# Performance work log

Hardware: AMD Instinct MI355X
Metric: run time of the kernel (lower is better)

Reference implementation:

```python
import jax, jax.numpy as jnp
from jax import lax
import numpy as np

B, C, H, W = 8, 192, 56, 56
N = H * W
K_CLUSTERS = 16   # num_centroids
K_NBRS = 9        # kNN neighbors
FACTOR = 2
COUT = C * FACTOR # hidden channels of graph conv
CPE_K = 7         # depthwise CPE kernel (odd)


def setup_inputs() -> dict:
    key = jax.random.key(0)
    ks = jax.random.split(key, 12)
    s = 0.02
    return {
        "x": jax.random.normal(ks[0], (B, C, H, W), jnp.float32),
        "labels": jax.random.randint(ks[1], (B, N), 0, K_CLUSTERS, jnp.int32),
        "cpe_w": jax.random.normal(ks[2], (C, 1, CPE_K, CPE_K), jnp.float32) * s,
        "cpe_b": jnp.zeros((C,), jnp.float32),
        "fc1_w": jax.random.normal(ks[3], (C, C), jnp.float32) * s,
        "fc1_b": jnp.zeros((C,), jnp.float32),
        "nn_v_w": jax.random.normal(ks[4], (2 * C, COUT), jnp.float32) * s,
        "nn_v_b": jnp.zeros((COUT,), jnp.float32),
        "nn_c_w": jax.random.normal(ks[5], (2 * C, COUT), jnp.float32) * s,
        "nn_c_b": jnp.zeros((COUT,), jnp.float32),
        "fc2_w": jax.random.normal(ks[6], (COUT, C), jnp.float32) * s,
        "fc2_b": jnp.zeros((C,), jnp.float32),
    }


def reference(x, labels, cpe_w, cpe_b, fc1_w, fc1_b, nn_v_w, nn_v_b,
              nn_c_w, nn_c_b, fc2_w, fc2_b):
    Bx, Cx, Hx, Wx = x.shape
    n = Hx * Wx
    shortcut = x
    # --- Conditional Position Encoding: depthwise conv + residual ---
    pe = lax.conv_general_dilated(
        x, cpe_w, (1, 1), "SAME", feature_group_count=Cx,
        dimension_numbers=("NCHW", "OIHW", "NCHW"))
    x = pe + cpe_b[None, :, None, None] + x
    # --- fc1: 1x1 conv ---
    xf = jnp.einsum("bchw,cd->bdhw", x, fc1_w) + fc1_b[None, :, None, None]
    xn = xf.reshape(Bx, Cx, n).transpose(0, 2, 1)  # [B,N,C]
    # --- organize_and_map: stable sort nodes by cluster label ---
    order = jnp.argsort(labels, axis=1)            # sorted pos -> orig idx (stable)
    mapping = jnp.argsort(order, axis=1)           # orig idx -> sorted pos
    xs = jnp.take_along_axis(xn, order[:, :, None], axis=1)  # [B,N,C]
    ls = jnp.take_along_axis(labels, order, axis=1)          # [B,N]
    # --- kNN on l2-normalized feats, restricted to same cluster ---
    xe = xs / jnp.maximum(jnp.linalg.norm(xs, axis=-1, keepdims=True), 1e-12)
    sq = jnp.sum(xe * xe, axis=-1)                 # [B,N]
    d2 = sq[:, :, None] + sq[:, None, :] - 2.0 * jnp.einsum("bnc,bmc->bnm", xe, xe)
    same = ls[:, :, None] == ls[:, None, :]        # [B,N,N] cluster mask
    d2 = jnp.where(same, d2, jnp.inf)
    _, nbr = lax.top_k(-d2, K_NBRS)                # [B,N,k] nearest in-cluster
    valid = jnp.take_along_axis(same, nbr, axis=2) # False when cluster < k
    # --- vertex edge conv: max_j MLP([x_i, x_j - x_i]) ---
    xj = jax.vmap(lambda xb, nb: xb[nb])(xs, nbr)  # [B,N,k,C]
    xi = xs[:, :, None, :]
    msg = jnp.concatenate([jnp.broadcast_to(xi, xj.shape), xj - xi], axis=-1)
    h = jax.nn.gelu(msg @ nn_v_w + nn_v_b)         # [B,N,k,COUT]
    h = jnp.where(valid[..., None], h, -jnp.inf)   # self is always valid
    hv = jnp.max(h, axis=2)                        # [B,N,COUT]
    # --- centroid edge conv over cluster centers (fully connected per image) ---
    onehot = (ls[:, :, None] == jnp.arange(K_CLUSTERS)[None, None, :]).astype(xs.dtype)
    cnt = jnp.maximum(onehot.sum(axis=1), 1.0)     # [B,K]
    cen = jnp.einsum("bnk,bnc->bkc", onehot, xs) / cnt[:, :, None]
    ci = cen[:, :, None, :]
    cj = cen[:, None, :, :]
    cmsg = jnp.concatenate(
        [jnp.broadcast_to(ci, (Bx, K_CLUSTERS, K_CLUSTERS, Cx)), cj - ci], axis=-1)
    hc = jnp.max(jax.nn.gelu(cmsg @ nn_c_w + nn_c_b), axis=2)  # [B,K,COUT]
    hcn = jax.vmap(lambda hb, lb: hb[lb])(hc, ls)  # scatter center feat to nodes
    hn = hv + hcn                                  # [B,N,COUT]
    # --- unshuffle back to original raster order ---
    out_nodes = jnp.take_along_axis(hn, mapping[:, :, None], axis=1)
    # --- fc2: 1x1 conv back to C, residual ---
    y = out_nodes @ fc2_w + fc2_b                  # [B,N,C]
    y = y.transpose(0, 2, 1).reshape(Bx, Cx, Hx, Wx)
    return y + shortcut
```

## Files before the change

kernel.cpp:

```cpp
#include <hip/hip_runtime.h>
#include <math.h>

#define NB 8
#define NC 192
#define NH 56
#define NW 56
#define NN 3136
#define NK 16
#define KNB 9
#define NCOUT 384
#define LPMAX 320
#define DSTRIDE 320
#define DSLOT (320 * 320)

#define FLT_INF __builtin_inff()

typedef short s16x8 __attribute__((ext_vector_type(8)));
typedef _Float16 f16x8 __attribute__((ext_vector_type(8)));
typedef float f32x4 __attribute__((ext_vector_type(4)));
typedef unsigned short us8 __attribute__((ext_vector_type(8)));
typedef unsigned short us4 __attribute__((ext_vector_type(4)));

__device__ __forceinline__ float gelu_t(float x) {
    const float k0 = 0.7978845608028654f;
    float u = k0 * (x + 0.044715f * x * x * x);
    float t = tanhf(u);
    return 0.5f * x * (1.0f + t);
}

__device__ __forceinline__ unsigned short f2bf(float f) {
    unsigned u = __float_as_uint(f);
    u += 0x7fff + ((u >> 16) & 1);
    return (unsigned short)(u >> 16);
}

__device__ __forceinline__ float bf2f(unsigned short h) {
    return __uint_as_float(((unsigned)h) << 16);
}

__global__ void order_kernel(const int* __restrict__ labels, int* __restrict__ order,
                             int* __restrict__ mapping, int* __restrict__ lsv,
                             int* __restrict__ cntk, int* __restrict__ offk) {
    int b = blockIdx.x >> 4;
    int k = blockIdx.x & 15;
    int lane = threadIdx.x;
    const int* lb = labels + (size_t)b * NN;
    int cntLess = 0, cntEq = 0;
    for (int n0 = 0; n0 < NN; n0 += 64) {
        int lab = lb[n0 + lane] & 15;
        cntLess += __popcll(__ballot(lab < k));
        cntEq += __popcll(__ballot(lab == k));
    }
    int base = cntLess;
    int run = 0;
    for (int n0 = 0; n0 < NN; n0 += 64) {
        int n = n0 + lane;
        int lab = lb[n] & 15;
        bool p = (lab == k);
        unsigned long long mask = __ballot(p);
        int rank = __popcll(mask & ((1ull << lane) - 1ull));
        if (p) {
            int pos = base + run + rank;
            order[b * NN + pos] = n;
            mapping[b * NN + n] = pos;
            lsv[b * NN + pos] = k;
        }
        run += __popcll(mask);
    }
    if (lane == 0) {
        offk[b * NK + k] = base;
        cntk[b * NK + k] = cntEq;
    }
}

__global__ __launch_bounds__(256) void conv_kernel(const float* __restrict__ X,
                                                   const float* __restrict__ W7,
                                                   const float* __restrict__ bias,
                                                   unsigned short* __restrict__ xpe) {
    __shared__ float tile[62 * 62];
    __shared__ float wl[49];
    int bc = blockIdx.x;
    int c = bc % NC;
    const float* Xp = X + (size_t)bc * NN;
    int tid = threadIdx.x;
    if (tid < 49) wl[tid] = W7[(size_t)c * 49 + tid];
    for (int idx = tid; idx < 62 * 62; idx += 256) {
        int ty = idx / 62, tx = idx % 62;
        int gy = ty - 3, gx = tx - 3;
        float v = 0.0f;
        if (gy >= 0 && gy < NH && gx >= 0 && gx < NW) v = Xp[gy * NW + gx];
        tile[idx] = v;
    }
    __syncthreads();
    float cb = bias[c];
    for (int g = tid; g < (NN / 4); g += 256) {
        int y = g / (NW / 4), x0 = (g % (NW / 4)) * 4;
        float a0 = 0.f, a1 = 0.f, a2 = 0.f, a3 = 0.f;
#pragma unroll
        for (int dy = 0; dy < 7; ++dy) {
            const float* tr = &tile[(y + dy) * 62 + x0];
#pragma unroll
            for (int dx = 0; dx < 7; ++dx) {
                float wv = wl[dy * 7 + dx];
                a0 += tr[dx] * wv;
                a1 += tr[dx + 1] * wv;
                a2 += tr[dx + 2] * wv;
                a3 += tr[dx + 3] * wv;
            }
        }
        const float* rr = &tile[(y + 3) * 62 + x0 + 3];
        us4 o;
        o[0] = f2bf(a0 + cb + rr[0]);
        o[1] = f2bf(a1 + cb + rr[1]);
        o[2] = f2bf(a2 + cb + rr[2]);
        o[3] = f2bf(a3 + cb + rr[3]);
        *(us4*)(xpe + (size_t)bc * NN + y * NW + x0) = o;
    }
}

__global__ void wcvt_all_kernel(const float* __restrict__ Wf1, const float* __restrict__ Wv,
                                const float* __restrict__ Wf2, unsigned short* __restrict__ wf1,
                                unsigned short* __restrict__ wfpmq,
                                unsigned short* __restrict__ wfq,
                                unsigned short* __restrict__ wf2) {
    int z = blockIdx.z, nt = blockIdx.x, kc = blockIdx.y;
    const float* W;
    unsigned short* Bf;
    int ldw, rowoff, KC, NT;
    bool diff = false;
    if (z == 0) { W = Wf1; Bf = wf1; ldw = NC; rowoff = 0; KC = 6; NT = 3; }
    else if (z == 1) { W = Wv; Bf = wfpmq; ldw = NCOUT; rowoff = 0; KC = 6; NT = 6; diff = true; }
    else if (z == 2) { W = Wv; Bf = wfq; ldw = NCOUT; rowoff = NC; KC = 6; NT = 6; }
    else { W = Wf2; Bf = wf2; ldw = NC; rowoff = 0; KC = 12; NT = 3; }
    if (nt >= NT || kc >= KC) return;
    int tid = threadIdx.x;
    int c = tid >> 6, l = tid & 63;
    int n = l & 15, q = l >> 4;
    int col = nt * 64 + c * 16 + n;
    int krow = rowoff + kc * 32 + q * 8;
    unsigned short pack[8];
#pragma unroll
    for (int j = 0; j < 8; ++j) {
        float v = W[(size_t)(krow + j) * ldw + col];
        if (diff) v -= W[(size_t)(NC + krow + j) * ldw + col];
        pack[j] = f2bf(v);
    }
    *(us8*)(Bf + ((((size_t)nt * KC + kc) * 4 + c) * 64 + l) * 8) = *(const us8*)pack;
}

__global__ __launch_bounds__(256) void tcvt_kernel(const unsigned short* __restrict__ xpe,
                                                   unsigned short* __restrict__ Af) {
    __shared__ unsigned short t[32][72];
    int b = blockIdx.z, kc = blockIdx.y, n0 = blockIdx.x * 64;
    int tid = threadIdx.x;
    int cl = tid >> 3, nl = (tid & 7) * 8;
    const unsigned short* src = xpe + ((size_t)b * NC + kc * 32 + cl) * NN + n0 + nl;
    *(us8*)&t[cl][nl] = *(const us8*)src;
    __syncthreads();
    int w = tid >> 6, l = tid & 63;
    int m = l & 15, q = l >> 4;
    int nloc = w * 16 + m;
    unsigned short pack[8];
#pragma unroll
    for (int j = 0; j < 8; ++j) pack[j] = t[q * 8 + j][nloc];
    int sg = blockIdx.x * 4 + w;
    *(us8*)(Af + (size_t)b * NN * NC + (((size_t)sg * 6 + kc) * 64 + l) * 8) =
        *(const us8*)pack;
}

template <int KC>
__global__ __launch_bounds__(256) void gemm_mfma(const unsigned short* __restrict__ Af,
                                                 size_t aStride,
                                                 const unsigned short* __restrict__ Bf,
                                                 const float* __restrict__ bias,
                                                 float* __restrict__ C, size_t cStride,
                                                 int ldc, unsigned short* __restrict__ Cfrag,
                                                 const int* __restrict__ rowmap) {
    int b = blockIdx.z;
    int w = threadIdx.x >> 6, lane = threadIdx.x & 63;
    int sg = blockIdx.y * 4 + w;
    int n0 = blockIdx.x * 64;
    const unsigned short* Ap = Af + (size_t)b * aStride + ((size_t)sg * KC * 64 + lane) * 8;
    const unsigned short* Bp = Bf + ((size_t)blockIdx.x * KC * 256 + lane) * 8;
    f32x4 acc[4] = {};
#pragma unroll
    for (int kc = 0; kc < KC; ++kc) {
        s16x8 a = *(const s16x8*)(Ap + kc * 512);
#pragma unroll
        for (int c = 0; c < 4; ++c) {
            s16x8 bv = *(const s16x8*)(Bp + kc * 2048 + c * 512);
            acc[c] = __builtin_amdgcn_mfma_f32_16x16x32_bf16(a, bv, acc[c], 0, 0, 0);
        }
    }
    int col0 = lane & 15, rq = lane >> 4;
    float* Cb = C + (size_t)b * cStride;
    int kcd = ldc >> 5;
#pragma unroll
    for (int r = 0; r < 4; ++r) {
        int grow = sg * 16 + rq * 4 + r;
        int orow = rowmap ? rowmap[(size_t)b * NN + grow] : grow;
#pragma unroll
        for (int c = 0; c < 4; ++c) {
            int col = n0 + c * 16 + col0;
            float v = acc[c][r];
            if (bias) v += bias[col];
            Cb[(size_t)orow * ldc + col] = v;
            if (Cfrag) {
                int s2 = orow >> 4, m2 = orow & 15;
                int kc2 = col >> 5, q2 = (col >> 3) & 3, j2 = col & 7;
                Cfrag[(size_t)b * cStride +
                      (((size_t)s2 * kcd + kc2) * 64 + q2 * 16 + m2) * 8 + j2] = f2bf(v);
            }
        }
    }
}

template <int KC>
__global__ __launch_bounds__(256) void gemm_mfma_h(const unsigned short* __restrict__ Af,
                                                   size_t aStride,
                                                   const unsigned short* __restrict__ Bf,
                                                   unsigned short* __restrict__ C,
                                                   size_t cStride, int ldc) {
    int b = blockIdx.z;
    int w = threadIdx.x >> 6, lane = threadIdx.x & 63;
    int sg = blockIdx.y * 4 + w;
    int n0 = blockIdx.x * 64;
    const unsigned short* Ap = Af + (size_t)b * aStride + ((size_t)sg * KC * 64 + lane) * 8;
    const unsigned short* Bp = Bf + ((size_t)blockIdx.x * KC * 256 + lane) * 8;
    f32x4 acc[4] = {};
#pragma unroll
    for (int kc = 0; kc < KC; ++kc) {
        s16x8 a = *(const s16x8*)(Ap + kc * 512);
#pragma unroll
        for (int c = 0; c < 4; ++c) {
            s16x8 bv = *(const s16x8*)(Bp + kc * 2048 + c * 512);
            acc[c] = __builtin_amdgcn_mfma_f32_16x16x32_bf16(a, bv, acc[c], 0, 0, 0);
        }
    }
    int col0 = lane & 15, rq = lane >> 4;
    unsigned short* Cb = C + (size_t)b * cStride;
#pragma unroll
    for (int r = 0; r < 4; ++r) {
        int grow = sg * 16 + rq * 4 + r;
#pragma unroll
        for (int c = 0; c < 4; ++c) {
            int col = n0 + c * 16 + col0;
            Cb[(size_t)grow * ldc + col] = f2bf(acc[c][r]);
        }
    }
}

__global__ void norm_kernel(const float* __restrict__ xs, float* __restrict__ rinv,
                            float* __restrict__ sqv) {
    int row = blockIdx.x * 4 + (threadIdx.x >> 6);
    int lane = threadIdx.x & 63;
    const float* p = xs + (size_t)row * NC;
    float v0 = p[lane], v1 = p[lane + 64], v2 = p[lane + 128];
    float s = v0 * v0 + v1 * v1 + v2 * v2;
#pragma unroll
    for (int m = 32; m; m >>= 1) s += __shfl_xor(s, m, 64);
    float nrm = fmaxf(sqrtf(s), 1e-12f);
    float ri = 1.0f / nrm;
    float e0 = v0 * ri, e1 = v1 * ri, e2 = v2 * ri;
    float s2 = e0 * e0 + e1 * e1 + e2 * e2;
#pragma unroll
    for (int m = 32; m; m >>= 1) s2 += __shfl_xor(s2, m, 64);
    if (lane == 0) {
        rinv[row] = ri;
        sqv[row] = s2;
    }
}

__global__ __launch_bounds__(384) void xe_cvt_kernel(const float* __restrict__ xs,
                                                     const float* __restrict__ rinv,
                                                     const int* __restrict__ offk,
                                                     const int* __restrict__ cntk,
                                                     _Float16* __restrict__ xef) {
    int b = blockIdx.z, k = blockIdx.y, strip = blockIdx.x;
    int bk = b * NK + k;
    int base = offk[bk], L = cntk[bk];
    if (strip * 16 >= L) return;
    int kc = threadIdx.x >> 6, l = threadIdx.x & 63;
    int m = l & 15, q = l >> 4;
    int rl = strip * 16 + m;
    int row = base + (rl < L ? rl : L - 1);
    float rv = rinv[(size_t)b * NN + row];
    const float* src = xs + ((size_t)b * NN + row) * NC + kc * 32 + q * 8;
    float4 v0 = *(const float4*)src;
    float4 v1 = *(const float4*)(src + 4);
    f16x8 pack;
    pack[0] = (_Float16)(v0.x * rv);
    pack[1] = (_Float16)(v0.y * rv);
    pack[2] = (_Float16)(v0.z * rv);
    pack[3] = (_Float16)(v0.w * rv);
    pack[4] = (_Float16)(v1.x * rv);
    pack[5] = (_Float16)(v1.y * rv);
    pack[6] = (_Float16)(v1.z * rv);
    pack[7] = (_Float16)(v1.w * rv);
    *(f16x8*)(xef + (size_t)bk * (20 * 6 * 512) + (((size_t)strip * 6 + kc) * 64 + l) * 8) =
        pack;
}

__global__ __launch_bounds__(256) void gram_kernel(const _Float16* __restrict__ xef,
                                                   const float* __restrict__ sqv,
                                                   const int* __restrict__ offk,
                                                   const int* __restrict__ cntk,
                                                   float* __restrict__ D) {
    int bk = blockIdx.z;
    int b = bk >> 4;
    int base = offk[bk], L = cntk[bk];
    int ti = blockIdx.x, tj = blockIdx.y;
    if (ti * 64 >= L || tj * 64 >= L) return;
    int w = threadIdx.x >> 6, lane = threadIdx.x & 63;
    const _Float16* Xf = xef + (size_t)bk * (20 * 6 * 512);
    const _Float16* Ap = Xf + (((size_t)(ti * 4 + w) * 6) * 64 + lane) * 8;
    f32x4 acc[4] = {};
#pragma unroll
    for (int kc = 0; kc < 6; ++kc) {
        f16x8 a = *(const f16x8*)(Ap + kc * 512);
#pragma unroll
        for (int js = 0; js < 4; ++js) {
            f16x8 bv = *(const f16x8*)(Xf + (((size_t)(tj * 4 + js) * 6 + kc) * 64 + lane) * 8);
            acc[js] = __builtin_amdgcn_mfma_f32_16x16x32_f16(a, bv, acc[js], 0, 0, 0);
        }
    }
    float* Dr = D + (size_t)bk * DSLOT;
    const float* Sb = sqv + (size_t)b * NN + base;
    int col0 = lane & 15, rq = lane >> 4;
#pragma unroll
    for (int r = 0; r < 4; ++r) {
        int i = ti * 64 + w * 16 + rq * 4 + r;
        float si = Sb[i < L ? i : L - 1];
#pragma unroll
        for (int js = 0; js < 4; ++js) {
            int j = tj * 64 + js * 16 + col0;
            float sj = Sb[j < L ? j : L - 1];
            Dr[(size_t)i * DSTRIDE + j] = si + sj - 2.0f * acc[js][r];
        }
    }
}

#define LEXLT(da, ca, db, cb) ((da) < (db) || ((da) == (db) && (ca) < (cb)))
__global__ __launch_bounds__(256) void select9_kernel(const float* __restrict__ D,
                                                      const int* __restrict__ lsv,
                                                      const int* __restrict__ offk,
                                                      const int* __restrict__ cntk,
                                                      int* __restrict__ nbr) {
    int b = blockIdx.y;
    int r = blockIdx.x * 4 + (threadIdx.x >> 6);
    int lane = threadIdx.x & 63;
    int k = lsv[(size_t)b * NN + r];
    int bk = b * NK + k;
    int base = offk[bk], L = cntk[bk];
    int Lc = L < LPMAX ? L : LPMAX;
    const float* Dr = D + (size_t)bk * DSLOT + (size_t)(r - base) * DSTRIDE;
    float d0, d1, d2, d3, d4;
    int c0, c1, c2, c3, c4;
    c0 = lane;
    c1 = lane + 64;
    c2 = lane + 128;
    c3 = lane + 192;
    c4 = lane + 256;
    d0 = c0 < Lc ? Dr[c0] : FLT_INF;
    d1 = c1 < Lc ? Dr[c1] : FLT_INF;
    d2 = c2 < Lc ? Dr[c2] : FLT_INF;
    d3 = c3 < Lc ? Dr[c3] : FLT_INF;
    d4 = c4 < Lc ? Dr[c4] : FLT_INF;
#define CS(da, ca, db, cb)                  \
    if (LEXLT(db, cb, da, ca)) {            \
        float t = da; da = db; db = t;      \
        int u = ca; ca = cb; cb = u;        \
    }
    CS(d0, c0, d1, c1) CS(d3, c3, d4, c4) CS(d2, c2, d4, c4) CS(d2, c2, d3, c3)
    CS(d1, c1, d4, c4) CS(d0, c0, d3, c3) CS(d0, c0, d2, c2) CS(d1, c1, d3, c3)
    CS(d1, c1, d2, c2)
#undef CS
    size_t row = (size_t)b * NN + r;
    for (int q = 0; q < KNB; ++q) {
        float bd = d0;
        int bc = c0;
#pragma unroll
        for (int m = 32; m; m >>= 1) {
            float od = __shfl_xor(bd, m, 64);
            int oc = __shfl_xor(bc, m, 64);
            if (LEXLT(od, oc, bd, bc)) {
                bd = od;
                bc = oc;
            }
        }
        if (lane == 0) nbr[row * KNB + q] = base + bc;
        if (d0 == bd && c0 == bc) {
            d0 = d1; c0 = c1;
            d1 = d2; c1 = c2;
            d2 = d3; c2 = c3;
            d3 = d4; c3 = c4;
            d4 = FLT_INF; c4 = 0x7fffffff;
        }
    }
}

__global__ __launch_bounds__(768) void cen_kernel(const float* __restrict__ xs,
                                                  const int* __restrict__ offk,
                                                  const int* __restrict__ cntk,
                                                  float* __restrict__ cen) {
    __shared__ float part[4][NC];
    int bk = blockIdx.x;
    int b = bk >> 4;
    int base = offk[bk], L = cntk[bk];
    int w = threadIdx.x / NC;
    int c = threadIdx.x % NC;
    const float* Xb = xs + ((size_t)b * NN + base) * NC + c;
    float s = 0.0f;
    for (int r = w; r < L; r += 4) s += Xb[(size_t)r * NC];
    part[w][c] = s;
    __syncthreads();
    if (threadIdx.x < NC) {
        int cc = threadIdx.x;
        float tot = part[0][cc] + part[1][cc] + part[2][cc] + part[3][cc];
        cen[(size_t)bk * NC + cc] = tot / fmaxf((float)L, 1.0f);
    }
}

__global__ __launch_bounds__(384) void pcqc_kernel(const float* __restrict__ cen,
                                                   const float* __restrict__ Wc,
                                                   const float* __restrict__ bc,
                                                   float* __restrict__ Pc,
                                                   float* __restrict__ Qc) {
    __shared__ float ce[NC];
    int bk = blockIdx.x;
    int o = threadIdx.x;
    if (o < NC) ce[o] = cen[(size_t)bk * NC + o];
    __syncthreads();
    float pc = bc[o], qc = 0.0f;
    for (int c = 0; c < NC; ++c) {
        pc += ce[c] * Wc[(size_t)c * NCOUT + o];
        qc += ce[c] * Wc[(size_t)(NC + c) * NCOUT + o];
    }
    Pc[(size_t)bk * NCOUT + o] = pc;
    Qc[(size_t)bk * NCOUT + o] = qc;
}

__global__ __launch_bounds__(384) void hcmax_kernel(const float* __restrict__ Pc,
                                                    const float* __restrict__ Qc,
                                                    float* __restrict__ hc) {
    int b = blockIdx.x >> 4, i = blockIdx.x & 15;
    int o = threadIdx.x;
    float pi = Pc[((size_t)b * NK + i) * NCOUT + o];
    float qi = Qc[((size_t)b * NK + i) * NCOUT + o];
    float pmq = pi - qi;
    float qmn = FLT_INF, qmx = -FLT_INF;
    for (int j = 0; j < NK; ++j) {
        float v = Qc[((size_t)b * NK + j) * NCOUT + o];
        qmn = fminf(qmn, v);
        qmx = fmaxf(qmx, v);
    }
    hc[((size_t)b * NK + i) * NCOUT + o] =
        fmaxf(gelu_t(pmq + qmn), gelu_t(pmq + qmx));
}

__global__ __launch_bounds__(256) void hv_kernel(const float* __restrict__ PmQ,
                                                 const unsigned short* __restrict__ Qh,
                                                 const int* __restrict__ nbr,
                                                 const int* __restrict__ lsv,
                                                 const float* __restrict__ hc,
                                                 unsigned short* __restrict__ hnf) {
    __shared__ float hnv[4][NCOUT];
    int b = blockIdx.y;
    int w = threadIdx.x >> 6, lane = threadIdx.x & 63;
    int i = blockIdx.x * 4 + w;
    size_t row = (size_t)b * NN + i;
    const float* Pr = PmQ + row * NCOUT;
    int lab = lsv[row];
    const float* hcr = hc + ((size_t)b * NK + lab) * NCOUT;
    int jn[KNB];
#pragma unroll
    for (int q = 0; q < KNB; ++q) jn[q] = nbr[row * KNB + q];
    const unsigned short* Qbb = Qh + (size_t)b * NN * NCOUT;
#pragma unroll
    for (int u = 0; u < 6; ++u) {
        int o = lane + 64 * u;
        float pmq = Pr[o];
        float q0 = bf2f(Qbb[(size_t)jn[0] * NCOUT + o]);
        float qmn = q0, qmx = q0;
#pragma unroll
        for (int q = 1; q < KNB; ++q) {
            float v = bf2f(Qbb[(size_t)jn[q] * NCOUT + o]);
            qmn = fminf(qmn, v);
            qmx = fmaxf(qmx, v);
        }
        float m = fmaxf(gelu_t(pmq + qmn), gelu_t(pmq + qmx));
        hnv[w][o] = m + hcr[o];
    }
    __syncthreads();
    if (threadIdx.x < 192) {
        int rsub = threadIdx.x / 48, c = threadIdx.x % 48;
        int i2 = blockIdx.x * 4 + rsub;
        int s = i2 >> 4, mm = i2 & 15;
        unsigned short pack[8];
#pragma unroll
        for (int e = 0; e < 8; ++e) pack[e] = f2bf(hnv[rsub][c * 8 + e]);
        *(us8*)(hnf + (size_t)b * NN * NCOUT +
                (((size_t)s * 12 + (c >> 2)) * 64 + (c & 3) * 16 + mm) * 8) =
            *(const us8*)pack;
    }
}

__global__ void out_kernel(const float* __restrict__ T, const float* __restrict__ X,
                           float* __restrict__ Y) {
    __shared__ float t[32][33];
    int b = blockIdx.z;
    int n0 = blockIdx.y * 32, c0 = blockIdx.x * 32;
    int tx = threadIdx.x, ty = threadIdx.y;
#pragma unroll
    for (int q = 0; q < 4; ++q) {
        int n = n0 + ty + q * 8;
        t[ty + q * 8][tx] = T[((size_t)b * NN + n) * NC + c0 + tx];
    }
    __syncthreads();
#pragma unroll
    for (int q = 0; q < 4; ++q) {
        int c = c0 + ty + q * 8;
        size_t idx = ((size_t)b * NC + c) * NN + n0 + tx;
        Y[idx] = t[tx][ty + q * 8] + X[idx];
    }
}

extern "C" void kernel_launch(void* const* d_in, const int* in_sizes, int n_in, void* d_out,
                              int out_size, void* d_ws, size_t ws_size, hipStream_t stream) {
    const float* x = (const float*)d_in[0];
    const int* labels = (const int*)d_in[1];
    const float* cpe_w = (const float*)d_in[2];
    const float* cpe_b = (const float*)d_in[3];
    const float* fc1_w = (const float*)d_in[4];
    const float* fc1_b = (const float*)d_in[5];
    const float* nn_v_w = (const float*)d_in[6];
    const float* nn_v_b = (const float*)d_in[7];
    const float* nn_c_w = (const float*)d_in[8];
    const float* nn_c_b = (const float*)d_in[9];
    const float* fc2_w = (const float*)d_in[10];
    const float* fc2_b = (const float*)d_in[11];
    float* out = (float*)d_out;

    const size_t SZ_XS = (size_t)NB * NN * NC;
    const size_t SZ_P = (size_t)NB * NN * NCOUT;
    const size_t BN = (size_t)NB * NN;
    const size_t SZ_CEN = (size_t)NB * NK * NC;
    const size_t SZ_PC = (size_t)NB * NK * NCOUT;

    float* base = (float*)d_ws;
    float* xs = base;
    float* xpeRegion = xs + SZ_XS;
    float* Pb = xpeRegion + SZ_XS;
    float* Qb = Pb + SZ_P;
    float* rinv = Qb + SZ_P;
    float* sqv = rinv + BN;
    float* cen = sqv + BN;
    float* Pc = cen + SZ_CEN;
    float* Qc = Pc + SZ_PC;
    float* hcv = Qc + SZ_PC;
    int* order = (int*)(hcv + SZ_PC);
    int* mapping = order + BN;
    int* lsv = mapping + BN;
    int* nbrv = lsv + BN;
    int* cntk = nbrv + BN * KNB;
    int* offk = cntk + NB * NK;
    unsigned short* xpe = (unsigned short*)xpeRegion;
    float* Dbuf = Pb;
    unsigned short* Qh = (unsigned short*)Qb;
    unsigned short* frag = (unsigned short*)(offk + NB * NK);
    unsigned short* xpeT_frag = frag;
    unsigned short* xs_frag = frag + SZ_XS;
    unsigned short* hn_frag = frag;
    unsigned short* wf1 = frag + 2 * SZ_XS;
    unsigned short* wfpmq = wf1 + (size_t)NC * NC;
    unsigned short* wfq = wfpmq + (size_t)NC * NCOUT;
    unsigned short* wf2 = wfq + (size_t)NC * NCOUT;
    _Float16* xef = (_Float16*)(wf2 + (size_t)NCOUT * NC);

    order_kernel<<<NB * NK, 64, 0, stream>>>(labels, order, mapping, lsv, cntk, offk);
    wcvt_all_kernel<<<dim3(6, 12, 4), 256, 0, stream>>>(fc1_w, nn_v_w, fc2_w, wf1, wfpmq,
                                                        wfq, wf2);
    conv_kernel<<<NB * NC, 256, 0, stream>>>(x, cpe_w, cpe_b, xpe);
    tcvt_kernel<<<dim3(NN / 64, NC / 32, NB), 256, 0, stream>>>(xpe, xpeT_frag);
    gemm_mfma<6><<<dim3(NC / 64, NN / 64, NB), 256, 0, stream>>>(
        xpeT_frag, SZ_XS / NB, wf1, fc1_b, xs, (size_t)NN * NC, NC, xs_frag, mapping);
    norm_kernel<<<(NB * NN) / 4, 256, 0, stream>>>(xs, rinv, sqv);
    xe_cvt_kernel<<<dim3(LPMAX / 16, NK, NB), 384, 0, stream>>>(xs, rinv, offk, cntk, xef);
    gram_kernel<<<dim3(LPMAX / 64, LPMAX / 64, NB * NK), 256, 0, stream>>>(xef, sqv, offk,
                                                                           cntk, Dbuf);
    select9_kernel<<<dim3(NN / 4, NB), 256, 0, stream>>>(Dbuf, lsv, offk, cntk, nbrv);
    gemm_mfma<6><<<dim3(NCOUT / 64, NN / 64, NB), 256, 0, stream>>>(
        xs_frag, SZ_XS / NB, wfpmq, nn_v_b, Pb, (size_t)NN * NCOUT, NCOUT, nullptr, nullptr);
    gemm_mfma_h<6><<<dim3(NCOUT / 64, NN / 64, NB), 256, 0, stream>>>(
        xs_frag, SZ_XS / NB, wfq, Qh, (size_t)NN * NCOUT, NCOUT);
    cen_kernel<<<NB * NK, 768, 0, stream>>>(xs, offk, cntk, cen);
    pcqc_kernel<<<NB * NK, NCOUT, 0, stream>>>(cen, nn_c_w, nn_c_b, Pc, Qc);
    hcmax_kernel<<<NB * NK, NCOUT, 0, stream>>>(Pc, Qc, hcv);
    hv_kernel<<<dim3(NN / 4, NB), 256, 0, stream>>>(Pb, Qh, nbrv, lsv, hcv, hn_frag);
    gemm_mfma<12><<<dim3(NC / 64, NN / 64, NB), 256, 0, stream>>>(
        hn_frag, SZ_P / NB, wf2, fc2_b, xs, (size_t)NN * NC, NC, nullptr, order);
    out_kernel<<<dim3(NC / 32, NN / 32, NB), dim3(32, 8), 0, stream>>>(xs, x, out);
}
```

Measured before the change: 327.7 us.

## Fuse norm into xe_cvt, merge centroid kernels, store fc2 output as bf16

Drops the separate row-norm kernel. xe_cvt now computes each row's squared norm through a shared-memory reduction and writes sqv itself. The two centroid kernels (pcqc and hcmax) become one kernel per image that keeps all 16 centroid projections in registers. The fc2 GEMM now writes bf16 instead of fp32, halving the traffic into the final transpose kernel at some precision cost. The gram kernel skips stores for rows and columns past the cluster length. The merged centroid kernel launches only 8 blocks, so parallelism there drops.

```diff
diff --git a/kernel.cpp b/kernel.cpp
--- a/kernel.cpp
+++ b/kernel.cpp
@@ -250,32 +250,51 @@
     }
 }
 
-__global__ void norm_kernel(const float* __restrict__ xs, float* __restrict__ rinv,
-                            float* __restrict__ sqv) {
-    int row = blockIdx.x * 4 + (threadIdx.x >> 6);
-    int lane = threadIdx.x & 63;
-    const float* p = xs + (size_t)row * NC;
-    float v0 = p[lane], v1 = p[lane + 64], v2 = p[lane + 128];
-    float s = v0 * v0 + v1 * v1 + v2 * v2;
-#pragma unroll
-    for (int m = 32; m; m >>= 1) s += __shfl_xor(s, m, 64);
-    float nrm = fmaxf(sqrtf(s), 1e-12f);
-    float ri = 1.0f / nrm;
-    float e0 = v0 * ri, e1 = v1 * ri, e2 = v2 * ri;
-    float s2 = e0 * e0 + e1 * e1 + e2 * e2;
-#pragma unroll
-    for (int m = 32; m; m >>= 1) s2 += __shfl_xor(s2, m, 64);
-    if (lane == 0) {
-        rinv[row] = ri;
-        sqv[row] = s2;
+template <int KC>
+__global__ __launch_bounds__(256) void gemm_mfma_hb(const unsigned short* __restrict__ Af,
+                                                    size_t aStride,
+                                                    const unsigned short* __restrict__ Bf,
+                                                    const float* __restrict__ bias,
+                                                    unsigned short* __restrict__ C,
+                                                    size_t cStride, int ldc,
+                                                    const int* __restrict__ rowmap) {
+    int b = blockIdx.z;
+    int w = threadIdx.x >> 6, lane = threadIdx.x & 63;
+    int sg = blockIdx.y * 4 + w;
+    int n0 = blockIdx.x * 64;
+    const unsigned short* Ap = Af + (size_t)b * aStride + ((size_t)sg * KC * 64 + lane) * 8;
+    const unsigned short* Bp = Bf + ((size_t)blockIdx.x * KC * 256 + lane) * 8;
+    f32x4 acc[4] = {};
+#pragma unroll
+    for (int kc = 0; kc < KC; ++kc) {
+        s16x8 a = *(const s16x8*)(Ap + kc * 512);
+#pragma unroll
+        for (int c = 0; c < 4; ++c) {
+            s16x8 bv = *(const s16x8*)(Bp + kc * 2048 + c * 512);
+            acc[c] = __builtin_amdgcn_mfma_f32_16x16x32_bf16(a, bv, acc[c], 0, 0, 0);
+        }
+    }
+    int col0 = lane & 15, rq = lane >> 4;
+    unsigned short* Cb = C + (size_t)b * cStride;
+#pragma unroll
+    for (int r = 0; r < 4; ++r) {
+        int grow = sg * 16 + rq * 4 + r;
+        int orow = rowmap[(size_t)b * NN + grow];
+#pragma unroll
+        for (int c = 0; c < 4; ++c) {
+            int col = n0 + c * 16 + col0;
+            Cb[(size_t)orow * ldc + col] = f2bf(acc[c][r] + bias[col]);
+        }
     }
 }
 
 __global__ __launch_bounds__(384) void xe_cvt_kernel(const float* __restrict__ xs,
-                                                     const float* __restrict__ rinv,
                                                      const int* __restrict__ offk,
                                                      const int* __restrict__ cntk,
-                                                     _Float16* __restrict__ xef) {
+                                                     _Float16* __restrict__ xef,
+                                                     float* __restrict__ sqv) {
+    __shared__ float psum[16][25];
+    __shared__ float rloc[16];
     int b = blockIdx.z, k = blockIdx.y, strip = blockIdx.x;
     int bk = b * NK + k;
     int base = offk[bk], L = cntk[bk];
@@ -284,10 +303,25 @@
     int m = l & 15, q = l >> 4;
     int rl = strip * 16 + m;
     int row = base + (rl < L ? rl : L - 1);
-    float rv = rinv[(size_t)b * NN + row];
     const float* src = xs + ((size_t)b * NN + row) * NC + kc * 32 + q * 8;
     float4 v0 = *(const float4*)src;
     float4 v1 = *(const float4*)(src + 4);
+    float part = v0.x * v0.x + v0.y * v0.y + v0.z * v0.z + v0.w * v0.w + v1.x * v1.x +
+                 v1.y * v1.y + v1.z * v1.z + v1.w * v1.w;
+    psum[m][kc * 4 + q] = part;
+    __syncthreads();
+    if (threadIdx.x < 16) {
+        float s = 0.0f;
+#pragma unroll
+        for (int i2 = 0; i2 < 24; ++i2) s += psum[threadIdx.x][i2];
+        float nrm = fmaxf(sqrtf(s), 1e-12f);
+        float ri = 1.0f / nrm;
+        rloc[threadIdx.x] = ri;
+        if (strip * 16 + (int)threadIdx.x < L)
+            sqv[(size_t)b * NN + base + strip * 16 + threadIdx.x] = (s * ri) * ri;
+    }
+    __syncthreads();
+    float rv = rloc[m];
     f16x8 pack;
     pack[0] = (_Float16)(v0.x * rv);
     pack[1] = (_Float16)(v0.y * rv);
@@ -330,12 +364,12 @@
 #pragma unroll
     for (int r = 0; r < 4; ++r) {
         int i = ti * 64 + w * 16 + rq * 4 + r;
-        float si = Sb[i < L ? i : L - 1];
+        if (i >= L) continue;
+        float si = Sb[i];
 #pragma unroll
         for (int js = 0; js < 4; ++js) {
             int j = tj * 64 + js * 16 + col0;
-            float sj = Sb[j < L ? j : L - 1];
-            Dr[(size_t)i * DSTRIDE + j] = si + sj - 2.0f * acc[js][r];
+            if (j < L) Dr[(size_t)i * DSTRIDE + j] = si + Sb[j] - 2.0f * acc[js][r];
         }
     }
 }
@@ -421,41 +455,44 @@
     }
 }
 
-__global__ __launch_bounds__(384) void pcqc_kernel(const float* __restrict__ cen,
+__global__ __launch_bounds__(384) void pchc_kernel(const float* __restrict__ cen,
                                                    const float* __restrict__ Wc,
                                                    const float* __restrict__ bc,
-                                                   float* __restrict__ Pc,
-                                                   float* __restrict__ Qc) {
-    __shared__ float ce[NC];
-    int bk = blockIdx.x;
+                                                   float* __restrict__ hc) {
+    __shared__ float ce[NK * NC];
+    int b = blockIdx.x;
     int o = threadIdx.x;
-    if (o < NC) ce[o] = cen[(size_t)bk * NC + o];
-    __syncthreads();
-    float pc = bc[o], qc = 0.0f;
+    for (int idx = o; idx < NK * NC; idx += 384) ce[idx] = cen[(size_t)b * NK * NC + idx];
+    __syncthreads();
+    float bcv = bc[o];
+    float pc[NK], qc[NK];
+#pragma unroll
+    for (int k = 0; k < NK; ++k) {
+        pc[k] = bcv;
+        qc[k] = 0.0f;
+    }
     for (int c = 0; c < NC; ++c) {
-        pc += ce[c] * Wc[(size_t)c * NCOUT + o];
-        qc += ce[c] * Wc[(size_t)(NC + c) * NCOUT + o];
-    }
-    Pc[(size_t)bk * NCOUT + o] = pc;
-    Qc[(size_t)bk * NCOUT + o] = qc;
-}
-
-__global__ __launch_bounds__(384) void hcmax_kernel(const float* __restrict__ Pc,
-                                                    const float* __restrict__ Qc,
-                                                    float* __restrict__ hc) {
-    int b = blockIdx.x >> 4, i = blockIdx.x & 15;
-    int o = threadIdx.x;
-    float pi = Pc[((size_t)b * NK + i) * NCOUT + o];
-    float qi = Qc[((size_t)b * NK + i) * NCOUT + o];
-    float pmq = pi - qi;
-    float qmn = FLT_INF, qmx = -FLT_INF;
-    for (int j = 0; j < NK; ++j) {
-        float v = Qc[((size_t)b * NK + j) * NCOUT + o];
-        qmn = fminf(qmn, v);
-        qmx = fmaxf(qmx, v);
-    }
-    hc[((size_t)b * NK + i) * NCOUT + o] =
-        fmaxf(gelu_t(pmq + qmn), gelu_t(pmq + qmx));
+        float w1 = Wc[(size_t)c * NCOUT + o];
+        float w2 = Wc[(size_t)(NC + c) * NCOUT + o];
+#pragma unroll
+        for (int k = 0; k < NK; ++k) {
+            float cv = ce[k * NC + c];
+            pc[k] += cv * w1;
+            qc[k] += cv * w2;
+        }
+    }
+    float qmn = qc[0], qmx = qc[0];
+#pragma unroll
+    for (int k = 1; k < NK; ++k) {
+        qmn = fminf(qmn, qc[k]);
+        qmx = fmaxf(qmx, qc[k]);
+    }
+#pragma unroll
+    for (int i = 0; i < NK; ++i) {
+        float pmq = pc[i] - qc[i];
+        hc[((size_t)b * NK + i) * NCOUT + o] =
+            fmaxf(gelu_t(pmq + qmn), gelu_t(pmq + qmx));
+    }
 }
 
 __global__ __launch_bounds__(256) void hv_kernel(const float* __restrict__ PmQ,
@@ -505,7 +542,7 @@
     }
 }
 
-__global__ void out_kernel(const float* __restrict__ T, const float* __restrict__ X,
+__global__ void out_kernel(const unsigned short* __restrict__ T, const float* __restrict__ X,
                            float* __restrict__ Y) {
     __shared__ float t[32][33];
     int b = blockIdx.z;
@@ -514,7 +551,7 @@
 #pragma unroll
     for (int q = 0; q < 4; ++q) {
         int n = n0 + ty + q * 8;
-        t[ty + q * 8][tx] = T[((size_t)b * NN + n) * NC + c0 + tx];
+        t[ty + q * 8][tx] = bf2f(T[((size_t)b * NN + n) * NC + c0 + tx]);
     }
     __syncthreads();
 #pragma unroll
@@ -555,9 +592,7 @@
     float* rinv = Qb + SZ_P;
     float* sqv = rinv + BN;
     float* cen = sqv + BN;
-    float* Pc = cen + SZ_CEN;
-    float* Qc = Pc + SZ_PC;
-    float* hcv = Qc + SZ_PC;
+    float* hcv = cen + SZ_CEN;
     int* order = (int*)(hcv + SZ_PC);
     int* mapping = order + BN;
     int* lsv = mapping + BN;
@@ -567,6 +602,7 @@
     unsigned short* xpe = (unsigned short*)xpeRegion;
     float* Dbuf = Pb;
     unsigned short* Qh = (unsigned short*)Qb;
+    unsigned short* out_t = (unsigned short*)xs;
     unsigned short* frag = (unsigned short*)(offk + NB * NK);
     unsigned short* xpeT_frag = frag;
     unsigned short* xs_frag = frag + SZ_XS;
@@ -584,8 +620,7 @@
     tcvt_kernel<<<dim3(NN / 64, NC / 32, NB), 256, 0, stream>>>(xpe, xpeT_frag);
     gemm_mfma<6><<<dim3(NC / 64, NN / 64, NB), 256, 0, stream>>>(
         xpeT_frag, SZ_XS / NB, wf1, fc1_b, xs, (size_t)NN * NC, NC, xs_frag, mapping);
-    norm_kernel<<<(NB * NN) / 4, 256, 0, stream>>>(xs, rinv, sqv);
-    xe_cvt_kernel<<<dim3(LPMAX / 16, NK, NB), 384, 0, stream>>>(xs, rinv, offk, cntk, xef);
+    xe_cvt_kernel<<<dim3(LPMAX / 16, NK, NB), 384, 0, stream>>>(xs, offk, cntk, xef, sqv);
     gram_kernel<<<dim3(LPMAX / 64, LPMAX / 64, NB * NK), 256, 0, stream>>>(xef, sqv, offk,
                                                                            cntk, Dbuf);
     select9_kernel<<<dim3(NN / 4, NB), 256, 0, stream>>>(Dbuf, lsv, offk, cntk, nbrv);
@@ -594,10 +629,9 @@
     gemm_mfma_h<6><<<dim3(NCOUT / 64, NN / 64, NB), 256, 0, stream>>>(
         xs_frag, SZ_XS / NB, wfq, Qh, (size_t)NN * NCOUT, NCOUT);
     cen_kernel<<<NB * NK, 768, 0, stream>>>(xs, offk, cntk, cen);
-    pcqc_kernel<<<NB * NK, NCOUT, 0, stream>>>(cen, nn_c_w, nn_c_b, Pc, Qc);
-    hcmax_kernel<<<NB * NK, NCOUT, 0, stream>>>(Pc, Qc, hcv);
+    pchc_kernel<<<NB, 384, 0, stream>>>(cen, nn_c_w, nn_c_b, hcv);
     hv_kernel<<<dim3(NN / 4, NB), 256, 0, stream>>>(Pb, Qh, nbrv, lsv, hcv, hn_frag);
-    gemm_mfma<12><<<dim3(NC / 64, NN / 64, NB), 256, 0, stream>>>(
-        hn_frag, SZ_P / NB, wf2, fc2_b, xs, (size_t)NN * NC, NC, nullptr, order);
-    out_kernel<<<dim3(NC / 32, NN / 32, NB), dim3(32, 8), 0, stream>>>(xs, x, out);
-}
+    gemm_mfma_hb<12><<<dim3(NC / 64, NN / 64, NB), 256, 0, stream>>>(
+        hn_frag, SZ_P / NB, wf2, fc2_b, out_t, (size_t)NN * NC, NC, order);
+    out_kernel<<<dim3(NC / 32, NN / 32, NB), dim3(32, 8), 0, stream>>>(out_t, x, out);
+}
```

Result: slower. 349.7 us (+6.7%).
